# Optimization experiments

Measured on AMD Instinct MI355X. Metric: run time of the kernel, lower is better.

## Reference

```python
import jax, jax.numpy as jnp
import numpy as np
from jax import lax

DIM = 64
HEADS = 4
B, H, W = 4, 256, 256


def _conv(x, w, b, pad, groups=1):
    y = lax.conv_general_dilated(x, w, (1, 1), [(pad, pad), (pad, pad)],
                                 dimension_numbers=('NCHW', 'OIHW', 'NCHW'),
                                 feature_group_count=groups)
    return y + b[None, :, None, None]


def _ckbd_mask(h, w, anchor):
    ii = jnp.arange(h)[:, None]
    jj = jnp.arange(w)[None, :]
    par = (ii + jj) % 2
    return (par == 1) if anchor else (par == 0)


def ckbd_anchor(y):
    return y * _ckbd_mask(y.shape[2], y.shape[3], True)


def ckbd_nonanchor(y):
    return y * _ckbd_mask(y.shape[2], y.shape[3], False)


def anchor_squeeze(y):
    b, c, h, w = y.shape
    even = y[:, :, 0::2, 1::2]  # anchor cells on even rows
    odd = y[:, :, 1::2, 0::2]   # anchor cells on odd rows
    return jnp.stack([even, odd], axis=3).reshape(b, c, h, w // 2)


def nonanchor_squeeze(y):
    b, c, h, w = y.shape
    even = y[:, :, 0::2, 0::2]
    odd = y[:, :, 1::2, 1::2]
    return jnp.stack([even, odd], axis=3).reshape(b, c, h, w // 2)


def anchor_unsqueeze(y):
    b, c, h, wh = y.shape
    out = jnp.zeros((b, c, h, wh * 2), y.dtype)
    out = out.at[:, :, 0::2, 1::2].set(y[:, :, 0::2, :])
    out = out.at[:, :, 1::2, 0::2].set(y[:, :, 1::2, :])
    return out


def nonanchor_unsqueeze(y):
    b, c, h, wh = y.shape
    out = jnp.zeros((b, c, h, wh * 2), y.dtype)
    out = out.at[:, :, 0::2, 0::2].set(y[:, :, 0::2, :])
    out = out.at[:, :, 1::2, 1::2].set(y[:, :, 1::2, :])
    return out


def setup_inputs() -> dict:
    key = jax.random.key(0)
    ks = jax.random.split(key, 16)
    s = 0.05
    C = DIM
    nrm = lambda k, shp: jax.random.normal(k, shp, jnp.float32) * s
    z = lambda n: jnp.zeros((n,), jnp.float32)
    return {
        'x1': jax.random.normal(ks[0], (B, C, H, W), jnp.float32),
        'x2': jax.random.normal(ks[1], (B, C, H, W), jnp.float32),
        'q1_w': nrm(ks[2], (C, C, 1, 1)), 'q1_b': z(C),
        'q2_w': nrm(ks[3], (C, 1, 3, 3)), 'q2_b': z(C),
        'k1_w': nrm(ks[4], (C, C, 1, 1)), 'k1_b': z(C),
        'k2_w': nrm(ks[5], (C, 1, 3, 3)), 'k2_b': z(C),
        'v1_w': nrm(ks[6], (C, C, 1, 1)), 'v1_b': z(C),
        'v2_w': nrm(ks[7], (C, 1, 3, 3)), 'v2_b': z(C),
        'r_w': nrm(ks[8], (2 * C, C, 5, 5)), 'r_b': z(2 * C),
        'm1_w': nrm(ks[9], (4 * C, 2 * C, 1, 1)), 'm1_b': z(4 * C),
        'm2_w': nrm(ks[10], (4 * C, 1, 3, 3)), 'm2_b': z(4 * C),
        'm3_w': nrm(ks[11], (2 * C, 4 * C, 1, 1)), 'm3_b': z(2 * C),
    }


def reference(x1, x2, q1_w, q1_b, q2_w, q2_b, k1_w, k1_b, k2_w, k2_b,
              v1_w, v1_b, v2_w, v2_b, r_w, r_b,
              m1_w, m1_b, m2_w, m2_b, m3_w, m3_b):
    C = DIM
    b, _, h, w = x1.shape
    d = C // HEADS
    x1_ac = ckbd_anchor(x1)
    x1_na = ckbd_nonanchor(x1)
    # QKV: 1x1 conv then depthwise 3x3
    q = _conv(_conv(x1_na, q1_w, q1_b, 0), q2_w, q2_b, 1, groups=C)
    k = _conv(_conv(x1_ac, k1_w, k1_b, 0), k2_w, k2_b, 1, groups=C)
    v = _conv(_conv(x2, v1_w, v1_b, 0), v2_w, v2_b, 1, groups=C)
    q = nonanchor_squeeze(q)  # (b, C, h, w//2)
    k = anchor_squeeze(k)
    v = anchor_squeeze(v)
    # per-head softmaxes: key over spatial, query over head channels
    kh = k.reshape(b, HEADS, d, h * (w // 2))
    qh = q.reshape(b, HEADS, d, h, w // 2)
    kh = jax.nn.softmax(kh, axis=-1).reshape(b, HEADS, d, h, w // 2)
    qh = jax.nn.softmax(qh, axis=2)
    vh = v.reshape(b, HEADS, d, h, w // 2)
    # scatter back to full grid (zeros off-pattern), flatten spatial
    kf = anchor_unsqueeze(kh.reshape(b, C, h, w // 2)).reshape(b, HEADS, d, h * w)
    vf = anchor_unsqueeze(vh.reshape(b, C, h, w // 2)).reshape(b, HEADS, d, h * w)
    qf = nonanchor_unsqueeze(qh.reshape(b, C, h, w // 2)).reshape(b, HEADS, d, h * w)
    # linear attention: context = K @ V^T (d x d), out = context^T @ Q
    ctx = jnp.einsum('bhdn,bhen->bhde', kf, vf)
    att = jnp.einsum('bhde,bhdn->bhen', ctx, qf).reshape(b, C, h, w)
    attention = _conv(att, r_w, r_b, 2)
    m = jax.nn.gelu(_conv(attention, m1_w, m1_b, 0), approximate=False)
    m = jax.nn.gelu(_conv(m, m2_w, m2_b, 1, groups=4 * C), approximate=False)
    m = _conv(m, m3_w, m3_b, 0)
    return attention + m
```

## Files before the change

### kernel.cpp

```cpp
#include <hip/hip_runtime.h>
#include <hip/hip_bf16.h>
#include <cstdint>

#define NHW 65536
#define NSQ 32768

static constexpr size_t OFF_AQ  = 0;
static constexpr size_t OFF_AK  = 8388608;
static constexpr size_t OFF_AV  = 16777216;
static constexpr size_t OFF_EK  = 33554432;
static constexpr size_t OFF_VD  = 41943040;
static constexpr size_t OFF_ATT = 50331648;
static constexpr size_t OFF_CTX = 58720256;
static constexpr size_t OFF_Z   = 58724352;
static constexpr size_t OFF_RWT = 58724608;
static constexpr size_t MB2_US  = 67108864;
static constexpr size_t A16_US  = 67108864;
static constexpr size_t W6_US   = 117654016;

typedef __attribute__((ext_vector_type(8))) short short8;
typedef __attribute__((ext_vector_type(4))) float floatx4;

__device__ __constant__ int TKH[25] = {0,0,0,1,1,2,2,2,3,3,4,4,4,  0,0,1,1,1,2,2,3,3,3,4,4};
__device__ __constant__ int TKW[25] = {0,2,4,1,3,0,2,4,1,3,0,2,4,  1,3,0,2,4,1,3,0,2,4,1,3};

__device__ __forceinline__ float geluf(float x) {
  return 0.5f * x * (1.0f + erff(x * 0.70710678118654752440f));
}
__device__ __forceinline__ unsigned short f2bf(float f) {
  union { float f; uint32_t u; } v; v.f = f;
  uint32_t x = v.u;
  uint32_t r = x + 0x7fffu + ((x >> 16) & 1u);
  return (unsigned short)(r >> 16);
}
__device__ __forceinline__ float bf2f(unsigned short u) {
  union { uint32_t i; float f; } v; v.i = ((uint32_t)u) << 16; return v.f;
}

__global__ void __launch_bounds__(256) k0_wprep(const float* __restrict__ rw,
                                                unsigned short* __restrict__ wAu) {
  int idx = blockIdx.x * 256 + threadIdx.x;
  int cj = idx & 7, o = (idx >> 3) & 127, chunk = (idx >> 10) & 7, tap = idx >> 13;
  int c = chunk * 8 + cj;
  int t = TKH[tap] * 5 + TKW[tap];
  wAu[idx] = f2bf(rw[(o * 64 + c) * 25 + t]);
}

__global__ void __launch_bounds__(256) k0b_w6(const float* __restrict__ m1w,
                                              unsigned short* __restrict__ w6) {
  int idx = blockIdx.x * 256 + threadIdx.x;
  int cj = idx & 7, o = (idx >> 3) & 255, chunk = idx >> 11;
  w6[idx] = f2bf(m1w[o * 128 + chunk * 8 + cj]);
}

__global__ void __launch_bounds__(256) k1_qkv(
    const float* __restrict__ x1, const float* __restrict__ x2,
    const float* __restrict__ q1w, const float* __restrict__ q1b,
    const float* __restrict__ k1w, const float* __restrict__ k1b,
    const float* __restrict__ v1w, const float* __restrict__ v1b,
    float* ws) {
  __shared__ float wq[4096], wk[4096], wv[4096];
  int tid = threadIdx.x;
  for (int idx = tid; idx < 4096; idx += 256) {
    int o = idx >> 6, c = idx & 63;
    wq[c * 64 + o] = q1w[o * 64 + c];
    wk[c * 64 + o] = k1w[o * 64 + c];
    wv[c * 64 + o] = v1w[o * 64 + c];
  }
  __syncthreads();
  int b = blockIdx.x >> 8, i = blockIdx.x & 255;
  int w = tid >> 6, l = tid & 63;
  int j = (((w >> 1) * 64 + l) << 1) | (w & 1);
  int par = (i + j) & 1;
  const float* wsel = par ? wk : wq;
  const float* bsel = par ? k1b : q1b;
  float acc[64];
#pragma unroll
  for (int o = 0; o < 64; o++) acc[o] = bsel[o];
  const float* xp = x1 + ((size_t)b * 64) * NHW + i * 256 + j;
  for (int c = 0; c < 64; c++) {
    float v = xp[(size_t)c * NHW];
    const float* wr = wsel + c * 64;
#pragma unroll
    for (int o = 0; o < 64; o++) acc[o] += wr[o] * v;
  }
  {
    float* dst = ws + (par ? OFF_AK : OFF_AQ) + ((size_t)b * 64) * NSQ + i * 128 + (j >> 1);
#pragma unroll
    for (int o = 0; o < 64; o++) dst[(size_t)o * NSQ] = acc[o];
  }
#pragma unroll
  for (int o = 0; o < 64; o++) acc[o] = v1b[o];
  const float* xp2 = x2 + ((size_t)b * 64) * NHW + i * 256 + j;
  for (int c = 0; c < 64; c++) {
    float v = xp2[(size_t)c * NHW];
    const float* wr = wv + c * 64;
#pragma unroll
    for (int o = 0; o < 64; o++) acc[o] += wr[o] * v;
  }
  float* dv = ws + OFF_AV + ((size_t)b * 64) * NHW + i * 256 + j;
#pragma unroll
  for (int o = 0; o < 64; o++) dv[(size_t)o * NHW] = acc[o];
}

__global__ void __launch_bounds__(256) k2_dw(
    float* ws,
    const float* __restrict__ kw2, const float* __restrict__ kb2, const float* __restrict__ kb1,
    const float* __restrict__ vw2, const float* __restrict__ vb2) {
  int bid = blockIdx.x;
  int b = bid >> 13, c = (bid >> 7) & 63, ip = bid & 127;
  int tid = threadIdx.x;
  int i = ip * 2 + (tid >> 7);
  int jp = tid & 127;
  int s = 1 - (i & 1);
  int j = 2 * jp + s;
  const float* AK = ws + OFF_AK + ((size_t)(b * 64 + c)) * NSQ;
  const float* w9 = kw2 + c * 9;
  float acc = kb2[c] + w9[4] * AK[i * 128 + jp];
  int cl = jp - 1 + s, cr = jp + s;
  if (i > 0) {
    const float* r = AK + (i - 1) * 128;
    if (cl >= 0)   acc += w9[0] * r[cl];
    if (cr <= 127) acc += w9[2] * r[cr];
  }
  if (i < 255) {
    const float* r = AK + (i + 1) * 128;
    if (cl >= 0)   acc += w9[6] * r[cl];
    if (cr <= 127) acc += w9[8] * r[cr];
  }
  float bs = 0.f;
  if (i > 0)   bs += w9[1];
  if (i < 255) bs += w9[7];
  if (j > 0)   bs += w9[3];
  if (j < 255) bs += w9[5];
  acc += kb1[c] * bs;
  float ek = expf(acc);
  ws[OFF_EK + ((size_t)(b * 64 + c)) * NSQ + i * 128 + jp] = ek;

  const float* AV = ws + OFF_AV + ((size_t)(b * 64 + c)) * NHW;
  const float* vw = vw2 + c * 9;
  float av = vb2[c];
#pragma unroll
  for (int kh = 0; kh < 3; kh++) {
    int r = i - 1 + kh;
    if (r < 0 || r > 255) continue;
    const float* rp = AV + r * 256;
#pragma unroll
    for (int kwd = 0; kwd < 3; kwd++) {
      int u = j - 1 + kwd;
      if (u < 0 || u > 255) continue;
      av += vw[kh * 3 + kwd] * rp[u];
    }
  }
  ws[OFF_VD + ((size_t)(b * 64 + c)) * NSQ + i * 128 + jp] = av;

  __shared__ float red[256];
  red[tid] = ek;
  __syncthreads();
#pragma unroll
  for (int off = 128; off > 0; off >>= 1) {
    if (tid < off) red[tid] += red[tid + off];
    __syncthreads();
  }
  if (tid == 0) atomicAdd(ws + OFF_Z + (b * 64 + c), red[0]);
}

__global__ void __launch_bounds__(256) k3_ctx(float* ws) {
  int bid = blockIdx.x;
  int b = bid >> 5, h = (bid >> 3) & 3, ch = bid & 7;
  int n0 = ch * 4096;
  int tid = threadIdx.x;
  int d = tid >> 4, e = tid & 15;
  __shared__ float ekt[16][260];
  __shared__ float vdt[16][260];
  const float* ekb = ws + OFF_EK + ((size_t)(b * 64 + h * 16)) * NSQ + n0;
  const float* vdb = ws + OFF_VD + ((size_t)(b * 64 + h * 16)) * NSQ + n0;
  float acc = 0.f;
  for (int sub = 0; sub < 16; sub++) {
    __syncthreads();
#pragma unroll
    for (int r = 0; r < 16; r++) {
      ekt[r][tid] = ekb[(size_t)r * NSQ + sub * 256 + tid];
      vdt[r][tid] = vdb[(size_t)r * NSQ + sub * 256 + tid];
    }
    __syncthreads();
#pragma unroll 8
    for (int x = 0; x < 256; x++) acc += ekt[d][x] * vdt[e][x];
  }
  atomicAdd(ws + OFF_CTX + ((b * 4 + h) * 16 + d) * 16 + e, acc);
}

__global__ void __launch_bounds__(256) k4_att(
    float* ws,
    const float* __restrict__ qw2, const float* __restrict__ qb2, const float* __restrict__ qb1) {
  int b = blockIdx.x >> 7, ip = blockIdx.x & 127;
  int tid = threadIdx.x;
  int i = ip * 2 + (tid >> 7);
  int jp = tid & 127;
  __shared__ float ctxn[1024];
  for (int idx = tid; idx < 1024; idx += 256)
    ctxn[idx] = ws[OFF_CTX + b * 1024 + idx] / ws[OFF_Z + b * 64 + (idx >> 4)];
  __syncthreads();
  int s = i & 1;
  int j = 2 * jp + s;
  int cl = jp - 1 + s, cr = jp + s;
  unsigned short* attB = (unsigned short*)(ws + OFF_ATT);
  unsigned short* dstp = attB + (((size_t)(b * 256 + i)) * 128 + jp) * 64;
  for (int h = 0; h < 4; h++) {
    float qv[16];
#pragma unroll
    for (int dc = 0; dc < 16; dc++) {
      int c = h * 16 + dc;
      const float* AQ = ws + OFF_AQ + ((size_t)(b * 64 + c)) * NSQ;
      const float* w9 = qw2 + c * 9;
      float acc = qb2[c] + w9[4] * AQ[i * 128 + jp];
      if (i > 0) {
        const float* r = AQ + (i - 1) * 128;
        if (cl >= 0)   acc += w9[0] * r[cl];
        if (cr <= 127) acc += w9[2] * r[cr];
      }
      if (i < 255) {
        const float* r = AQ + (i + 1) * 128;
        if (cl >= 0)   acc += w9[6] * r[cl];
        if (cr <= 127) acc += w9[8] * r[cr];
      }
      float bs = 0.f;
      if (i > 0)   bs += w9[1];
      if (i < 255) bs += w9[7];
      if (j > 0)   bs += w9[3];
      if (j < 255) bs += w9[5];
      qv[dc] = acc + qb1[c] * bs;
    }
    float mx = qv[0];
#pragma unroll
    for (int dc = 1; dc < 16; dc++) mx = fmaxf(mx, qv[dc]);
    float sum = 0.f;
#pragma unroll
    for (int dc = 0; dc < 16; dc++) { qv[dc] = expf(qv[dc] - mx); sum += qv[dc]; }
    float inv = 1.0f / sum;
#pragma unroll
    for (int e = 0; e < 16; e++) {
      float a = 0.f;
#pragma unroll
      for (int dc = 0; dc < 16; dc++) a += ctxn[h * 256 + dc * 16 + e] * qv[dc];
      dstp[h * 16 + e] = f2bf(a * inv);
    }
  }
}

__global__ void __launch_bounds__(256) k5_mfma(
    const unsigned short* __restrict__ attB, const unsigned short* __restrict__ wAu,
    const float* __restrict__ rb, float* __restrict__ out,
    unsigned short* __restrict__ a16) {
  int p = blockIdx.y, b = blockIdx.z;
  int i0 = (blockIdx.x >> 2) * 4;
  int jp0 = (blockIdx.x & 3) * 32;
  int tid = threadIdx.x;
  int wv = tid >> 6, lane = tid & 63;
  int mh = wv & 1, nh = wv >> 1;
  int l15 = lane & 15, quad = lane >> 4;

  __shared__ __align__(16) unsigned short attL[24576];
  __shared__ __align__(16) unsigned short wL[8192];

  const unsigned short* attBase = attB + ((size_t)b * 256) * 128 * 64;
  for (int k = 0; k < 12; k++) {
    int u = k * 256 + tid;
    int chunk = u & 7;
    int pos = (u >> 3) & 15;
    int cbr = u >> 7;
    int cb = cbr % 3, lr = cbr / 3;
    int r = i0 - 2 + lr;
    int jp = jp0 - 2 + cb * 16 + pos;
    short8 v = {0, 0, 0, 0, 0, 0, 0, 0};
    if (r >= 0 && r < 256 && jp >= 0 && jp < 128)
      v = *(const short8*)(attBase + (((size_t)r * 128) + jp) * 64 + chunk * 8);
    int slot = chunk ^ (pos & 7);
    *(short8*)(attL + (((size_t)cbr * 16 + pos) * 8 + slot) * 8) = v;
  }

  floatx4 acc[16];
#pragma unroll
  for (int x = 0; x < 16; x++) acc[x] = floatx4{0.f, 0.f, 0.f, 0.f};

  int riv[4], ci2[4];
#pragma unroll
  for (int nt = 0; nt < 4; nt++) {
    int ntg = nh * 4 + nt;
    riv[nt] = ntg >> 1;
    ci2[nt] = (ntg & 1) * 16 + l15 + 2;
  }

  int t0 = p ? 13 : 0;
  int ntaps = p ? 12 : 13;
  for (int tt = 0; tt < ntaps; tt++) {
    int tap = t0 + tt;
    int kh = TKH[tap], kw = TKW[tap];
    __syncthreads();
    {
      const short8* src = (const short8*)(wAu + (size_t)tap * 8192);
      short8* dst = (short8*)wL;
#pragma unroll
      for (int k = 0; k < 4; k++) dst[k * 256 + tid] = src[k * 256 + tid];
    }
    __syncthreads();
#pragma unroll
    for (int chalf = 0; chalf < 2; chalf++) {
      short8 a[4], bf[4];
#pragma unroll
      for (int mt = 0; mt < 4; mt++)
        a[mt] = *(const short8*)(wL + (((chalf * 4 + quad) * 128) + mh * 64 + mt * 16 + l15) * 8);
#pragma unroll
      for (int nt = 0; nt < 4; nt++) {
        int lr = riv[nt] + kh;
        int off = ((kw - 2) + ((p + riv[nt]) & 1) - ((riv[nt] + kh) & 1)) >> 1;
        int lc = ci2[nt] + off;
        int cb = lc >> 4, pos = lc & 15;
        int slot = (chalf * 4 + quad) ^ (pos & 7);
        bf[nt] = *(const short8*)(attL + ((((lr * 3 + cb) * 16 + pos) * 8) + slot) * 8);
      }
#pragma unroll
      for (int mt = 0; mt < 4; mt++)
#pragma unroll
        for (int nt = 0; nt < 4; nt++)
          acc[mt * 4 + nt] =
              __builtin_amdgcn_mfma_f32_16x16x32_bf16(a[mt], bf[nt], acc[mt * 4 + nt], 0, 0, 0);
    }
  }

#pragma unroll
  for (int mt = 0; mt < 4; mt++) {
#pragma unroll
    for (int nt = 0; nt < 4; nt++) {
      int ntg = nh * 4 + nt;
      int i = i0 + (ntg >> 1);
      int jp = jp0 + (ntg & 1) * 16 + l15;
      int j = 2 * jp + ((p + i) & 1);
      floatx4 v = acc[mt * 4 + nt];
      int o0 = mh * 64 + mt * 16 + quad * 4;
      ushort4 u4;
      float r0 = v[0] + rb[o0 + 0];
      float r1 = v[1] + rb[o0 + 1];
      float r2 = v[2] + rb[o0 + 2];
      float r3 = v[3] + rb[o0 + 3];
      out[(((size_t)(b * 128 + o0 + 0)) * 256 + i) * 256 + j] = r0;
      out[(((size_t)(b * 128 + o0 + 1)) * 256 + i) * 256 + j] = r1;
      out[(((size_t)(b * 128 + o0 + 2)) * 256 + i) * 256 + j] = r2;
      out[(((size_t)(b * 128 + o0 + 3)) * 256 + i) * 256 + j] = r3;
      u4.x = f2bf(r0); u4.y = f2bf(r1); u4.z = f2bf(r2); u4.w = f2bf(r3);
      *(ushort4*)(a16 + ((size_t)b * 65536 + (size_t)i * 256 + j) * 128 + o0) = u4;
    }
  }
}

__global__ void __launch_bounds__(256) k6_m1(
    const unsigned short* __restrict__ a16, const unsigned short* __restrict__ w6,
    const float* __restrict__ m1b, unsigned short* __restrict__ mb) {
  int px0 = blockIdx.x * 128;
  int og = blockIdx.y, b = blockIdx.z;
  int tid = threadIdx.x;
  int wv = tid >> 6, lane = tid & 63;
  int mh = wv & 1, nh = wv >> 1;
  int l15 = lane & 15, quad = lane >> 4;
  __shared__ __align__(16) unsigned short attL[16384];

  const unsigned short* src = a16 + ((size_t)b * 65536 + px0) * 128;
#pragma unroll
  for (int k = 0; k < 8; k++) {
    int u = k * 256 + tid;
    int n = u >> 4, chunk = u & 15;
    short8 v = *(const short8*)(src + (size_t)n * 128 + chunk * 8);
    int slot = chunk ^ (n & 7);
    *(short8*)(attL + ((size_t)n * 16 + slot) * 8) = v;
  }
  __syncthreads();

  floatx4 acc[16];
#pragma unroll
  for (int x = 0; x < 16; x++) acc[x] = floatx4{0.f, 0.f, 0.f, 0.f};

#pragma unroll
  for (int step = 0; step < 4; step++) {
    int chunk = step * 4 + quad;
    short8 a[4], bw[4];
#pragma unroll
    for (int mt = 0; mt < 4; mt++) {
      int row = mh * 64 + mt * 16 + l15;
      int slot = chunk ^ (row & 7);
      a[mt] = *(const short8*)(attL + (row * 16 + slot) * 8);
    }
#pragma unroll
    for (int nt = 0; nt < 4; nt++) {
      int o = og * 128 + nh * 64 + nt * 16 + l15;
      bw[nt] = *(const short8*)(w6 + ((size_t)chunk * 256 + o) * 8);
    }
#pragma unroll
    for (int mt = 0; mt < 4; mt++)
#pragma unroll
      for (int nt = 0; nt < 4; nt++)
        acc[mt * 4 + nt] =
            __builtin_amdgcn_mfma_f32_16x16x32_bf16(a[mt], bw[nt], acc[mt * 4 + nt], 0, 0, 0);
  }

#pragma unroll
  for (int nt = 0; nt < 4; nt++) {
    int o = og * 128 + nh * 64 + nt * 16 + l15;
    float bo = m1b[o];
#pragma unroll
    for (int mt = 0; mt < 4; mt++) {
      int px = px0 + mh * 64 + mt * 16 + quad * 4;
      floatx4 v = acc[mt * 4 + nt];
      ushort4 u;
      u.x = f2bf(geluf(v[0] + bo));
      u.y = f2bf(geluf(v[1] + bo));
      u.z = f2bf(geluf(v[2] + bo));
      u.w = f2bf(geluf(v[3] + bo));
      *(ushort4*)(mb + ((size_t)(b * 256 + o)) * NHW + px) = u;
    }
  }
}

__global__ void __launch_bounds__(256) k7_m2(
    const unsigned short* __restrict__ mb, const float* __restrict__ m2w,
    const float* __restrict__ m2b, unsigned short* __restrict__ mb2) {
  int b = blockIdx.z;
  int c = blockIdx.y;
  int band = blockIdx.x;
  int tid = threadIdx.x;
  int cs = tid & 31;
  int rr = tid >> 5;
  int j0 = cs * 8;
  int r0 = band * 32 + rr * 4;
  const unsigned short* base = mb + ((size_t)(b * 256 + c)) * NHW;
  unsigned short* obase = mb2 + ((size_t)(b * 256 + c)) * NHW;

  float w9[9];
#pragma unroll
  for (int t = 0; t < 9; t++) w9[t] = m2w[c * 9 + t];
  float bias = m2b[c];

  float f[6][10];
#pragma unroll
  for (int rowi = 0; rowi < 6; rowi++) {
    int r = r0 - 1 + rowi;
    short8 v = {0, 0, 0, 0, 0, 0, 0, 0};
    unsigned short lft = 0, rgt = 0;
    if (r >= 0 && r < 256) {
      v = *(const short8*)(base + r * 256 + j0);
      if (j0 > 0)       lft = base[r * 256 + j0 - 1];
      if (j0 + 8 < 256) rgt = base[r * 256 + j0 + 8];
    }
    f[rowi][0] = bf2f(lft);
#pragma unroll
    for (int x = 0; x < 8; x++) f[rowi][1 + x] = bf2f((unsigned short)v[x]);
    f[rowi][9] = bf2f(rgt);
  }

#pragma unroll
  for (int ri = 0; ri < 4; ri++) {
    float acc[8];
#pragma unroll
    for (int jj = 0; jj < 8; jj++) acc[jj] = bias;
#pragma unroll
    for (int kh = 0; kh < 3; kh++) {
#pragma unroll
      for (int kw = 0; kw < 3; kw++) {
        float wv = w9[kh * 3 + kw];
#pragma unroll
        for (int jj = 0; jj < 8; jj++) acc[jj] += wv * f[ri + kh][jj + kw];
      }
    }
    short8 o;
#pragma unroll
    for (int jj = 0; jj < 8; jj++) o[jj] = (short)f2bf(geluf(acc[jj]));
    *(short8*)(obase + (r0 + ri) * 256 + j0) = o;
  }
}

__global__ void __launch_bounds__(256) k8_m3(
    const unsigned short* __restrict__ mb2, const float* __restrict__ m3w,
    const float* __restrict__ m3b, float* __restrict__ out) {
  int n0 = blockIdx.x * 64;
  int og = blockIdx.y, b = blockIdx.z;
  int tid = threadIdx.x;
  int ot = tid >> 4, pt = tid & 15;
  __shared__ __align__(16) float aL[2048];
  __shared__ __align__(16) float wL[32 * 68];
  float acc[4][4];
#pragma unroll
  for (int x = 0; x < 4; x++)
#pragma unroll
    for (int y = 0; y < 4; y++) acc[x][y] = 0.f;
  for (int cc = 0; cc < 256; cc += 32) {
    __syncthreads();
#pragma unroll
    for (int k = 0; k < 2; k++) {
      int e4 = (k * 256 + tid) * 4;
      int ci = e4 >> 6, p0 = e4 & 63;
      const ushort4 uv = *(const ushort4*)(mb2 + ((size_t)(b * 256 + cc + ci)) * NHW + n0 + p0);
      aL[ci * 64 + p0 + 0] = bf2f(uv.x);
      aL[ci * 64 + p0 + 1] = bf2f(uv.y);
      aL[ci * 64 + p0 + 2] = bf2f(uv.z);
      aL[ci * 64 + p0 + 3] = bf2f(uv.w);
    }
#pragma unroll
    for (int k = 0; k < 8; k++) {
      int idx = k * 256 + tid;
      int o = idx >> 5, ci2 = idx & 31;
      wL[ci2 * 68 + o] = m3w[(og * 64 + o) * 256 + cc + ci2];
    }
    __syncthreads();
    for (int ci = 0; ci < 32; ci++) {
      float4 a4 = *(const float4*)(aL + ci * 64 + pt * 4);
      float4 w4 = *(const float4*)(wL + ci * 68 + ot * 4);
      acc[0][0] += w4.x * a4.x; acc[0][1] += w4.x * a4.y; acc[0][2] += w4.x * a4.z; acc[0][3] += w4.x * a4.w;
      acc[1][0] += w4.y * a4.x; acc[1][1] += w4.y * a4.y; acc[1][2] += w4.y * a4.z; acc[1][3] += w4.y * a4.w;
      acc[2][0] += w4.z * a4.x; acc[2][1] += w4.z * a4.y; acc[2][2] += w4.z * a4.z; acc[2][3] += w4.z * a4.w;
      acc[3][0] += w4.w * a4.x; acc[3][1] += w4.w * a4.y; acc[3][2] += w4.w * a4.z; acc[3][3] += w4.w * a4.w;
    }
  }
#pragma unroll
  for (int oi = 0; oi < 4; oi++) {
    int o = og * 64 + ot * 4 + oi;
    float bo = m3b[o];
    size_t addr = ((size_t)(b * 128 + o)) * NHW + n0 + pt * 4;
    float4 prev = *(const float4*)(out + addr);
    float4 res;
    res.x = prev.x + acc[oi][0] + bo;
    res.y = prev.y + acc[oi][1] + bo;
    res.z = prev.z + acc[oi][2] + bo;
    res.w = prev.w + acc[oi][3] + bo;
    *(float4*)(out + addr) = res;
  }
}

extern "C" void kernel_launch(void* const* d_in, const int* in_sizes, int n_in,
                              void* d_out, int out_size, void* d_ws, size_t ws_size,
                              hipStream_t stream) {
  const float* x1  = (const float*)d_in[0];
  const float* x2  = (const float*)d_in[1];
  const float* q1w = (const float*)d_in[2];  const float* q1b = (const float*)d_in[3];
  const float* q2w = (const float*)d_in[4];  const float* q2b = (const float*)d_in[5];
  const float* k1w = (const float*)d_in[6];  const float* k1b = (const float*)d_in[7];
  const float* k2w = (const float*)d_in[8];  const float* k2b = (const float*)d_in[9];
  const float* v1w = (const float*)d_in[10]; const float* v1b = (const float*)d_in[11];
  const float* v2w = (const float*)d_in[12]; const float* v2b = (const float*)d_in[13];
  const float* rw  = (const float*)d_in[14]; const float* rb  = (const float*)d_in[15];
  const float* m1w = (const float*)d_in[16]; const float* m1b = (const float*)d_in[17];
  const float* m2w = (const float*)d_in[18]; const float* m2b = (const float*)d_in[19];
  const float* m3w = (const float*)d_in[20]; const float* m3b = (const float*)d_in[21];
  float* ws = (float*)d_ws;
  float* out = (float*)d_out;
  unsigned short* mb  = (unsigned short*)d_ws;
  unsigned short* mb2 = (unsigned short*)d_ws + MB2_US;
  unsigned short* a16 = (unsigned short*)d_ws + A16_US;
  unsigned short* w6  = (unsigned short*)d_ws + W6_US;
  unsigned short* attB = (unsigned short*)(ws + OFF_ATT);
  unsigned short* wAu  = (unsigned short*)(ws + OFF_RWT);

  (void)hipMemsetAsync((char*)d_ws + OFF_CTX * sizeof(float), 0, (4096 + 256) * sizeof(float), stream);
  k0_wprep<<<800, 256, 0, stream>>>(rw, wAu);
  k0b_w6<<<128, 256, 0, stream>>>(m1w, w6);
  k1_qkv<<<1024, 256, 0, stream>>>(x1, x2, q1w, q1b, k1w, k1b, v1w, v1b, ws);
  k2_dw<<<32768, 256, 0, stream>>>(ws, k2w, k2b, k1b, v2w, v2b);
  k3_ctx<<<128, 256, 0, stream>>>(ws);
  k4_att<<<512, 256, 0, stream>>>(ws, q2w, q2b, q1b);
  k5_mfma<<<dim3(256, 2, 4), 256, 0, stream>>>(attB, wAu, rb, out, a16);
  k6_m1<<<dim3(512, 2, 4), 256, 0, stream>>>(a16, w6, m1b, mb);
  k7_m2<<<dim3(8, 256, 4), 256, 0, stream>>>(mb, m2w, m2b, mb2);
  k8_m3<<<dim3(1024, 2, 4), 256, 0, stream>>>(mb2, m3w, m3b, out);
}
```

Before: 1.129 ms.

## Switch MLP hidden activations to channel-last and move m3 conv to bf16 MFMA

k6 now writes the 256-channel GELU hidden tensor in pixel-major (NHWC) order by swapping the MFMA operand roles. k7's depthwise 3x3 is rewritten to walk along rows with a sliding register window, each thread owning 4 contiguous channels. k8, the 1x1 projection from 256 to 128 channels, is rebuilt as a bf16 MFMA GEMM using a pre-converted weight buffer from a new k0c_w8 kernel, replacing the fp32 FMA tile loop. This trades the scalar fp32 GEMM cost for tensor-core work, but adds bf16 weight rounding and strided scalar read-modify-write stores to the output. It also reuses workspace offset 0, which previously held mb, for the new weights.

Measured after the change: 1.091 ms. 1.03x faster.

```diff
diff --git a/kernel.cpp b/kernel.cpp
--- a/kernel.cpp
+++ b/kernel.cpp
@@ -17,6 +17,7 @@
 static constexpr size_t MB2_US  = 67108864;
 static constexpr size_t A16_US  = 67108864;
 static constexpr size_t W6_US   = 117654016;
+static constexpr size_t W8_US   = 0;
 
 typedef __attribute__((ext_vector_type(8))) short short8;
 typedef __attribute__((ext_vector_type(4))) float floatx4;
@@ -51,6 +52,13 @@
   int idx = blockIdx.x * 256 + threadIdx.x;
   int cj = idx & 7, o = (idx >> 3) & 255, chunk = idx >> 11;
   w6[idx] = f2bf(m1w[o * 128 + chunk * 8 + cj]);
+}
+
+__global__ void __launch_bounds__(256) k0c_w8(const float* __restrict__ m3w,
+                                              unsigned short* __restrict__ w8) {
+  int idx = blockIdx.x * 256 + threadIdx.x;
+  int cj = idx & 7, o = (idx >> 3) & 127, chunk = idx >> 10;
+  w8[idx] = f2bf(m3w[o * 256 + chunk * 8 + cj]);
 }
 
 __global__ void __launch_bounds__(256) k1_qkv(
@@ -382,40 +390,40 @@
 #pragma unroll
   for (int step = 0; step < 4; step++) {
     int chunk = step * 4 + quad;
-    short8 a[4], bw[4];
+    short8 aw[4], bp[4];
 #pragma unroll
     for (int mt = 0; mt < 4; mt++) {
-      int row = mh * 64 + mt * 16 + l15;
+      int o = og * 128 + mh * 64 + mt * 16 + l15;
+      aw[mt] = *(const short8*)(w6 + ((size_t)chunk * 256 + o) * 8);
+    }
+#pragma unroll
+    for (int nt = 0; nt < 4; nt++) {
+      int row = nh * 64 + nt * 16 + l15;
       int slot = chunk ^ (row & 7);
-      a[mt] = *(const short8*)(attL + (row * 16 + slot) * 8);
-    }
-#pragma unroll
-    for (int nt = 0; nt < 4; nt++) {
-      int o = og * 128 + nh * 64 + nt * 16 + l15;
-      bw[nt] = *(const short8*)(w6 + ((size_t)chunk * 256 + o) * 8);
+      bp[nt] = *(const short8*)(attL + (row * 16 + slot) * 8);
     }
 #pragma unroll
     for (int mt = 0; mt < 4; mt++)
 #pragma unroll
       for (int nt = 0; nt < 4; nt++)
         acc[mt * 4 + nt] =
-            __builtin_amdgcn_mfma_f32_16x16x32_bf16(a[mt], bw[nt], acc[mt * 4 + nt], 0, 0, 0);
-  }
-
-#pragma unroll
-  for (int nt = 0; nt < 4; nt++) {
-    int o = og * 128 + nh * 64 + nt * 16 + l15;
-    float bo = m1b[o];
-#pragma unroll
-    for (int mt = 0; mt < 4; mt++) {
-      int px = px0 + mh * 64 + mt * 16 + quad * 4;
+            __builtin_amdgcn_mfma_f32_16x16x32_bf16(aw[mt], bp[nt], acc[mt * 4 + nt], 0, 0, 0);
+  }
+
+#pragma unroll
+  for (int mt = 0; mt < 4; mt++) {
+    int o0 = og * 128 + mh * 64 + mt * 16 + quad * 4;
+    float4 bo = *(const float4*)(m1b + o0);
+#pragma unroll
+    for (int nt = 0; nt < 4; nt++) {
+      int px = px0 + nh * 64 + nt * 16 + l15;
       floatx4 v = acc[mt * 4 + nt];
       ushort4 u;
-      u.x = f2bf(geluf(v[0] + bo));
-      u.y = f2bf(geluf(v[1] + bo));
-      u.z = f2bf(geluf(v[2] + bo));
-      u.w = f2bf(geluf(v[3] + bo));
-      *(ushort4*)(mb + ((size_t)(b * 256 + o)) * NHW + px) = u;
+      u.x = f2bf(geluf(v[0] + bo.x));
+      u.y = f2bf(geluf(v[1] + bo.y));
+      u.z = f2bf(geluf(v[2] + bo.z));
+      u.w = f2bf(geluf(v[3] + bo.w));
+      *(ushort4*)(mb + ((size_t)b * 65536 + px) * 256 + o0) = u;
     }
   }
 }
@@ -423,114 +431,140 @@
 __global__ void __launch_bounds__(256) k7_m2(
     const unsigned short* __restrict__ mb, const float* __restrict__ m2w,
     const float* __restrict__ m2b, unsigned short* __restrict__ mb2) {
+  int b = blockIdx.y;
+  int i0 = (blockIdx.x >> 2) * 4;
+  int jq = blockIdx.x & 3;
+  int t = threadIdx.x;
+  int l = t & 63, ri = t >> 6;
+  int co = l * 4;
+  int i = i0 + ri;
+  int j0 = jq * 64;
+  const unsigned short* ibase = mb + ((size_t)b * 65536) * 256 + co;
+  unsigned short* obase = mb2 + ((size_t)b * 65536) * 256 + co;
+
+  float w[9][4], bias[4];
+#pragma unroll
+  for (int cc = 0; cc < 4; cc++) {
+    bias[cc] = m2b[co + cc];
+#pragma unroll
+    for (int tap = 0; tap < 9; tap++) w[tap][cc] = m2w[(co + cc) * 9 + tap];
+  }
+
+  float wA[3][4], wB[3][4], wC[3][4];
+
+#define K7_LOAD(dst, ir, jc)                                                        \
+  do {                                                                              \
+    if ((unsigned)(ir) < 256u && (unsigned)(jc) < 256u) {                           \
+      ushort4 u_ = *(const ushort4*)(ibase + ((size_t)((ir) * 256 + (jc))) * 256);  \
+      dst[0] = bf2f(u_.x); dst[1] = bf2f(u_.y);                                     \
+      dst[2] = bf2f(u_.z); dst[3] = bf2f(u_.w);                                     \
+    } else {                                                                        \
+      dst[0] = 0.f; dst[1] = 0.f; dst[2] = 0.f; dst[3] = 0.f;                       \
+    }                                                                               \
+  } while (0)
+
+#pragma unroll
+  for (int r = 0; r < 3; r++) {
+    K7_LOAD(wA[r], i - 1 + r, j0 - 1);
+    K7_LOAD(wB[r], i - 1 + r, j0);
+  }
+
+  for (int j = j0; j < j0 + 64; j++) {
+#pragma unroll
+    for (int r = 0; r < 3; r++) K7_LOAD(wC[r], i - 1 + r, j + 1);
+    float acc[4];
+#pragma unroll
+    for (int cc = 0; cc < 4; cc++) {
+      acc[cc] = bias[cc]
+        + w[0][cc] * wA[0][cc] + w[1][cc] * wB[0][cc] + w[2][cc] * wC[0][cc]
+        + w[3][cc] * wA[1][cc] + w[4][cc] * wB[1][cc] + w[5][cc] * wC[1][cc]
+        + w[6][cc] * wA[2][cc] + w[7][cc] * wB[2][cc] + w[8][cc] * wC[2][cc];
+    }
+    ushort4 u;
+    u.x = f2bf(geluf(acc[0]));
+    u.y = f2bf(geluf(acc[1]));
+    u.z = f2bf(geluf(acc[2]));
+    u.w = f2bf(geluf(acc[3]));
+    *(ushort4*)(obase + ((size_t)(i * 256 + j)) * 256) = u;
+#pragma unroll
+    for (int r = 0; r < 3; r++) {
+#pragma unroll
+      for (int cc = 0; cc < 4; cc++) { wA[r][cc] = wB[r][cc]; wB[r][cc] = wC[r][cc]; }
+    }
+  }
+#undef K7_LOAD
+}
+
+__global__ void __launch_bounds__(256) k8_m3(
+    const unsigned short* __restrict__ mb2, const unsigned short* __restrict__ w8,
+    const float* __restrict__ m3b, float* __restrict__ out) {
+  int px0 = blockIdx.x * 128;
   int b = blockIdx.z;
-  int c = blockIdx.y;
-  int band = blockIdx.x;
   int tid = threadIdx.x;
-  int cs = tid & 31;
-  int rr = tid >> 5;
-  int j0 = cs * 8;
-  int r0 = band * 32 + rr * 4;
-  const unsigned short* base = mb + ((size_t)(b * 256 + c)) * NHW;
-  unsigned short* obase = mb2 + ((size_t)(b * 256 + c)) * NHW;
-
-  float w9[9];
-#pragma unroll
-  for (int t = 0; t < 9; t++) w9[t] = m2w[c * 9 + t];
-  float bias = m2b[c];
-
-  float f[6][10];
-#pragma unroll
-  for (int rowi = 0; rowi < 6; rowi++) {
-    int r = r0 - 1 + rowi;
-    short8 v = {0, 0, 0, 0, 0, 0, 0, 0};
-    unsigned short lft = 0, rgt = 0;
-    if (r >= 0 && r < 256) {
-      v = *(const short8*)(base + r * 256 + j0);
-      if (j0 > 0)       lft = base[r * 256 + j0 - 1];
-      if (j0 + 8 < 256) rgt = base[r * 256 + j0 + 8];
-    }
-    f[rowi][0] = bf2f(lft);
-#pragma unroll
-    for (int x = 0; x < 8; x++) f[rowi][1 + x] = bf2f((unsigned short)v[x]);
-    f[rowi][9] = bf2f(rgt);
-  }
-
-#pragma unroll
-  for (int ri = 0; ri < 4; ri++) {
-    float acc[8];
-#pragma unroll
-    for (int jj = 0; jj < 8; jj++) acc[jj] = bias;
-#pragma unroll
-    for (int kh = 0; kh < 3; kh++) {
-#pragma unroll
-      for (int kw = 0; kw < 3; kw++) {
-        float wv = w9[kh * 3 + kw];
-#pragma unroll
-        for (int jj = 0; jj < 8; jj++) acc[jj] += wv * f[ri + kh][jj + kw];
+  int wv = tid >> 6, lane = tid & 63;
+  int mh = wv & 1, nh = wv >> 1;
+  int l15 = lane & 15, quad = lane >> 4;
+  __shared__ __align__(16) unsigned short attL[16384];
+
+  floatx4 acc[16];
+#pragma unroll
+  for (int x = 0; x < 16; x++) acc[x] = floatx4{0.f, 0.f, 0.f, 0.f};
+
+  for (int kk = 0; kk < 2; kk++) {
+    if (kk) __syncthreads();
+    const unsigned short* src = mb2 + ((size_t)b * 65536 + px0) * 256 + kk * 128;
+#pragma unroll
+    for (int k = 0; k < 8; k++) {
+      int u = k * 256 + tid;
+      int n = u >> 4, ch = u & 15;
+      short8 v = *(const short8*)(src + (size_t)n * 256 + ch * 8);
+      int slot = ch ^ (n & 7);
+      *(short8*)(attL + ((size_t)n * 16 + slot) * 8) = v;
+    }
+    __syncthreads();
+
+#pragma unroll
+    for (int step = 0; step < 4; step++) {
+      int ch = step * 4 + quad;
+      int chg = kk * 16 + ch;
+      short8 aw[4], bp[4];
+#pragma unroll
+      for (int mt = 0; mt < 4; mt++) {
+        int o = mh * 64 + mt * 16 + l15;
+        aw[mt] = *(const short8*)(w8 + ((size_t)chg * 128 + o) * 8);
       }
-    }
-    short8 o;
-#pragma unroll
-    for (int jj = 0; jj < 8; jj++) o[jj] = (short)f2bf(geluf(acc[jj]));
-    *(short8*)(obase + (r0 + ri) * 256 + j0) = o;
-  }
-}
-
-__global__ void __launch_bounds__(256) k8_m3(
-    const unsigned short* __restrict__ mb2, const float* __restrict__ m3w,
-    const float* __restrict__ m3b, float* __restrict__ out) {
-  int n0 = blockIdx.x * 64;
-  int og = blockIdx.y, b = blockIdx.z;
-  int tid = threadIdx.x;
-  int ot = tid >> 4, pt = tid & 15;
-  __shared__ __align__(16) float aL[2048];
-  __shared__ __align__(16) float wL[32 * 68];
-  float acc[4][4];
-#pragma unroll
-  for (int x = 0; x < 4; x++)
-#pragma unroll
-    for (int y = 0; y < 4; y++) acc[x][y] = 0.f;
-  for (int cc = 0; cc < 256; cc += 32) {
-    __syncthreads();
-#pragma unroll
-    for (int k = 0; k < 2; k++) {
-      int e4 = (k * 256 + tid) * 4;
-      int ci = e4 >> 6, p0 = e4 & 63;
-      const ushort4 uv = *(const ushort4*)(mb2 + ((size_t)(b * 256 + cc + ci)) * NHW + n0 + p0);
-      aL[ci * 64 + p0 + 0] = bf2f(uv.x);
-      aL[ci * 64 + p0 + 1] = bf2f(uv.y);
-      aL[ci * 64 + p0 + 2] = bf2f(uv.z);
-      aL[ci * 64 + p0 + 3] = bf2f(uv.w);
-    }
-#pragma unroll
-    for (int k = 0; k < 8; k++) {
-      int idx = k * 256 + tid;
-      int o = idx >> 5, ci2 = idx & 31;
-      wL[ci2 * 68 + o] = m3w[(og * 64 + o) * 256 + cc + ci2];
-    }
-    __syncthreads();
-    for (int ci = 0; ci < 32; ci++) {
-      float4 a4 = *(const float4*)(aL + ci * 64 + pt * 4);
-      float4 w4 = *(const float4*)(wL + ci * 68 + ot * 4);
-      acc[0][0] += w4.x * a4.x; acc[0][1] += w4.x * a4.y; acc[0][2] += w4.x * a4.z; acc[0][3] += w4.x * a4.w;
-      acc[1][0] += w4.y * a4.x; acc[1][1] += w4.y * a4.y; acc[1][2] += w4.y * a4.z; acc[1][3] += w4.y * a4.w;
-      acc[2][0] += w4.z * a4.x; acc[2][1] += w4.z * a4.y; acc[2][2] += w4.z * a4.z; acc[2][3] += w4.z * a4.w;
-      acc[3][0] += w4.w * a4.x; acc[3][1] += w4.w * a4.y; acc[3][2] += w4.w * a4.z; acc[3][3] += w4.w * a4.w;
-    }
-  }
-#pragma unroll
-  for (int oi = 0; oi < 4; oi++) {
-    int o = og * 64 + ot * 4 + oi;
-    float bo = m3b[o];
-    size_t addr = ((size_t)(b * 128 + o)) * NHW + n0 + pt * 4;
-    float4 prev = *(const float4*)(out + addr);
-    float4 res;
-    res.x = prev.x + acc[oi][0] + bo;
-    res.y = prev.y + acc[oi][1] + bo;
-    res.z = prev.z + acc[oi][2] + bo;
-    res.w = prev.w + acc[oi][3] + bo;
-    *(float4*)(out + addr) = res;
+#pragma unroll
+      for (int nt = 0; nt < 4; nt++) {
+        int row = nh * 64 + nt * 16 + l15;
+        int slot = ch ^ (row & 7);
+        bp[nt] = *(const short8*)(attL + (row * 16 + slot) * 8);
+      }
+#pragma unroll
+      for (int mt = 0; mt < 4; mt++)
+#pragma unroll
+        for (int nt = 0; nt < 4; nt++)
+          acc[mt * 4 + nt] =
+              __builtin_amdgcn_mfma_f32_16x16x32_bf16(aw[mt], bp[nt], acc[mt * 4 + nt], 0, 0, 0);
+    }
+  }
+
+#pragma unroll
+  for (int mt = 0; mt < 4; mt++) {
+    int o0 = mh * 64 + mt * 16 + quad * 4;
+    float4 bo = *(const float4*)(m3b + o0);
+#pragma unroll
+    for (int nt = 0; nt < 4; nt++) {
+      int px = px0 + nh * 64 + nt * 16 + l15;
+      floatx4 v = acc[mt * 4 + nt];
+      size_t a0 = ((size_t)(b * 128 + o0 + 0)) * NHW + px;
+      size_t a1 = ((size_t)(b * 128 + o0 + 1)) * NHW + px;
+      size_t a2 = ((size_t)(b * 128 + o0 + 2)) * NHW + px;
+      size_t a3 = ((size_t)(b * 128 + o0 + 3)) * NHW + px;
+      out[a0] += v[0] + bo.x;
+      out[a1] += v[1] + bo.y;
+      out[a2] += v[2] + bo.z;
+      out[a3] += v[3] + bo.w;
+    }
   }
 }
 
@@ -555,6 +589,7 @@
   unsigned short* mb2 = (unsigned short*)d_ws + MB2_US;
   unsigned short* a16 = (unsigned short*)d_ws + A16_US;
   unsigned short* w6  = (unsigned short*)d_ws + W6_US;
+  unsigned short* w8  = (unsigned short*)d_ws + W8_US;
   unsigned short* attB = (unsigned short*)(ws + OFF_ATT);
   unsigned short* wAu  = (unsigned short*)(ws + OFF_RWT);
 
@@ -567,6 +602,7 @@
   k4_att<<<512, 256, 0, stream>>>(ws, q2w, q2b, q1b);
   k5_mfma<<<dim3(256, 2, 4), 256, 0, stream>>>(attB, wAu, rb, out, a16);
   k6_m1<<<dim3(512, 2, 4), 256, 0, stream>>>(a16, w6, m1b, mb);
-  k7_m2<<<dim3(8, 256, 4), 256, 0, stream>>>(mb, m2w, m2b, mb2);
-  k8_m3<<<dim3(1024, 2, 4), 256, 0, stream>>>(mb2, m3w, m3b, out);
-}
+  k7_m2<<<dim3(256, 4), 256, 0, stream>>>(mb, m2w, m2b, mb2);
+  k0c_w8<<<128, 256, 0, stream>>>(m3w, w8);
+  k8_m3<<<dim3(512, 1, 4), 256, 0, stream>>>(mb2, w8, m3b, out);
+}
```
